# Optimization experiments

Measured on AMD Instinct MI355X. Metric: run time of the kernel, lower is better.

The kernel has to match this reference:

```python
import jax, jax.numpy as jnp
import numpy as np

# Dimensions
N = 50000      # num entities
FIN = 100      # entity input dim
NHID = 100     # per-head hidden dim
H = 2          # heads in first GAT layer
REL = 100      # relation embedding dim (== entity_out_dim[0])
E = 800000     # num edges
NRELS = 200    # num relations
B = 512        # batch of facts
HDIM = 100     # time-embedding dim (h_dim)
ALPHA = 0.2    # leaky relu slope


def l2norm(x, eps=1e-12):
    # torch F.normalize(p=2, dim=1)
    return x / jnp.maximum(jnp.linalg.norm(x, axis=1, keepdims=True), eps)


def gat_layer(x, edge0, edge1, rel_e, a, a2, num_nodes, concat):
    """KBAT SpGraphAttentionLayer (dropout omitted: eval mode).
    a: [out, 2*in + nrela]; a2: [out]. Aggregates into edge0 (edge[0])."""
    fin = x.shape[1]
    a_src, a_dst, a_rel = a[:, :fin], a[:, fin:2 * fin], a[:, 2 * fin:]
    # edge_m = a @ cat(h_src, h_dst, rel).T, computed without materializing the concat
    m = x[edge0] @ a_src.T + x[edge1] @ a_dst.T + rel_e @ a_rel.T  # [E, out]
    powers = -jax.nn.leaky_relu(m @ a2, ALPHA)                      # [E]
    e = jnp.exp(powers)                                             # [E]
    rowsum = jax.ops.segment_sum(e, edge0, num_segments=num_nodes) + 1e-12  # [N]
    h = jax.ops.segment_sum(e[:, None] * m, edge0, num_segments=num_nodes)  # [N, out]
    h = h / rowsum[:, None]
    return jax.nn.elu(h) if concat else h


def setup_inputs() -> dict:
    key = jax.random.key(0)
    ks = jax.random.split(key, 13)
    s = 0.08  # xavier-ish scale, keeps exp() of attention logits tame
    return {
        "entity_embeddings": jax.random.normal(ks[0], (N, FIN), jnp.float32) * s,
        "relation_table": jax.random.normal(ks[1], (NRELS, REL), jnp.float32) * s,
        "weight_t2": jax.random.normal(ks[2], (1, HDIM), jnp.float32),
        "bias_t2": jax.random.normal(ks[3], (1, HDIM), jnp.float32),
        "W_entities": jax.random.normal(ks[4], (FIN, H * NHID), jnp.float32) * s,
        "a_heads": jax.random.normal(ks[5], (H, NHID, 2 * FIN + REL), jnp.float32) * s,
        "a2_heads": jax.random.normal(ks[6], (H, NHID), jnp.float32) * s,
        "W_rel": jax.random.normal(ks[7], (REL, H * NHID), jnp.float32) * s,
        "a_out": jax.random.normal(ks[8], (H * NHID, 3 * H * NHID), jnp.float32) * s,
        "a2_out": jax.random.normal(ks[9], (H * NHID,), jnp.float32) * s,
        "edge_list": jax.random.randint(ks[10], (2, E), 0, N),
        "edge_type": jax.random.randint(ks[11], (E,), 0, NRELS),
        "batch_inputs": jax.random.randint(ks[12], (B, 4), 0, N),
    }


def reference(entity_embeddings, relation_table, weight_t2, bias_t2, W_entities,
              a_heads, a2_heads, W_rel, a_out, a2_out,
              edge_list, edge_type, batch_inputs):
    edge0, edge1 = edge_list[0], edge_list[1]
    # edge_embed = stack of relation_dict lookups
    edge_embed = relation_table[edge_type]                     # [E, REL]

    # SpGAT: multi-head attention layer 1 (concat=True, elu inside layer)
    heads = [gat_layer(entity_embeddings, edge0, edge1, edge_embed,
                       a_heads[i], a2_heads[i], N, True) for i in range(H)]
    x1 = jnp.concatenate(heads, axis=1)                        # [N, H*NHID]

    # NOTE: repo passes edge_embed (per-edge) as relation_embed -> [E, H*NHID]
    out_relation_1 = edge_embed @ W_rel                        # [E, H*NHID]
    edge_embed2 = out_relation_1[edge_type]                    # [E, H*NHID]

    x2 = jax.nn.elu(gat_layer(x1, edge0, edge1, edge_embed2, a_out, a2_out, N, False))

    # entity_embeddings.data = normalize(...).detach() happens before W_entities mm
    emb_norm = l2norm(entity_embeddings)

    # time embeddings: h_t rows are all identical -> index by heads is a broadcast
    t2 = batch_inputs[:, 3].astype(jnp.float32)                # [B]
    he = jnp.cos(t2[:, None] * weight_t2[0] + bias_t2[0])      # [B, HDIM]
    his_temp_embs = jnp.broadcast_to(he[:, None, :], (B, B, HDIM))

    mask = jnp.zeros((N,), x2.dtype).at[batch_inputs[:, 2]].set(1.0)
    entities_upgraded = emb_norm @ W_entities                  # [N, H*NHID]
    out = l2norm(entities_upgraded + mask[:, None] * x2)
    return out, his_temp_embs
```

## Files before the change

kernel.cpp:

```cpp
#include <hip/hip_runtime.h>
#include <hip/hip_fp16.h>
#include <stdint.h>

#define N_NODES 50000
#define FIN_D   100
#define E_EDGES 800000
#define NRELS   200
#define B_BATCH 512
#define HDIM    100

typedef _Float16 f16x8 __attribute__((ext_vector_type(8)));
typedef short    s16x8 __attribute__((ext_vector_type(8)));
typedef float    f32x4v __attribute__((ext_vector_type(4)));

__device__ __forceinline__ unsigned short f2bf(float f){
  unsigned int x = __builtin_bit_cast(unsigned int, f);
  unsigned int lsb = (x >> 16) & 1u;
  x += 0x7fffu + lsb;
  return (unsigned short)(x >> 16);
}
__device__ __forceinline__ float ldf(const void* p, size_t i, int fdt){
  if (fdt == 2) return __half2float(((const __half*)p)[i]);
  if (fdt == 1){ unsigned int x = ((unsigned int)((const unsigned short*)p)[i]) << 16;
                 return __builtin_bit_cast(float, x); }
  return ((const float*)p)[i];
}
__device__ __forceinline__ void stf(void* p, size_t i, float v, int fdt){
  if (fdt == 2) ((__half*)p)[i] = __float2half_rn(v);
  else if (fdt == 1) ((unsigned short*)p)[i] = f2bf(v);
  else ((float*)p)[i] = v;
}
__device__ __forceinline__ int ild(const void* p, size_t i, int i64){
  return i64 ? (int)((const long long*)p)[i] : ((const int*)p)[i];
}

__global__ void k_probe(const unsigned short* __restrict__ eh, const unsigned int* __restrict__ ew,
                        const unsigned int* __restrict__ elw, int* __restrict__ ifl){
  int t = threadIdx.x;
  int cF = 0, cB = 0, c32 = 0;
  #pragma unroll
  for (int j = 0; j < 4; ++j){
    unsigned short u = eh[4*t + j];
    {
      int e5 = (u >> 10) & 31, m = u & 1023;
      float v = (e5 == 0) ? ldexpf((float)m, -24) : ldexpf(1.f + m/1024.f, e5 - 15);
      if (v >= 0.004f && v <= 0.30f) cF++;
    }
    {
      unsigned int x = ((unsigned int)(u & 0x7FFF)) << 16;
      float v = __builtin_bit_cast(float, x);
      if (v >= 0.004f && v <= 0.30f) cB++;
    }
  }
  #pragma unroll
  for (int j = 0; j < 2; ++j){
    unsigned int w = ew[2*t + j] & 0x7FFFFFFFu;
    float v = __builtin_bit_cast(float, w);
    if (v >= 0.004f && v <= 0.30f) c32++;
  }
  for (int o = 1; o < 64; o <<= 1){
    cF += __shfl_xor(cF, o); cB += __shfl_xor(cB, o); c32 += __shfl_xor(c32, o);
  }
  int z = (elw[2*t + 1] == 0u) ? 1 : 0;
  unsigned long long mb = __ballot(z);
  if (t == 0){
    int fdt;
    if (c32 >= 96) fdt = 0;
    else fdt = (cB > cF) ? 1 : 2;
    ifl[1] = fdt;
    ifl[0] = (__popcll(mb) >= 60) ? 1 : 0;
  }
}

__global__ void k_init(int* __restrict__ midx, int* __restrict__ cnt,
                       int* __restrict__ nflag, int* __restrict__ fcnt){
  int i = blockIdx.x*256 + threadIdx.x;
  if (i < N_NODES){ midx[i] = -1; cnt[i] = 0; nflag[i] = 0; }
  if (i == 0) fcnt[0] = 0;
}
__global__ void k_mset(const void* __restrict__ binp, const int* __restrict__ ifl,
                       int* __restrict__ midx){
  int i = blockIdx.x*256 + threadIdx.x;
  if (i >= B_BATCH) return;
  midx[ild(binp, (size_t)i*4 + 2, ifl[0])] = i;
}

__global__ void k_tables(const void* __restrict__ ah, const void* __restrict__ aout,
                         const void* __restrict__ a2h, const void* __restrict__ a2o,
                         const void* __restrict__ went, const int* __restrict__ ifl,
                         float* __restrict__ aTs, float* __restrict__ aoTs,
                         float* __restrict__ a2f, float* __restrict__ a2of,
                         unsigned short* __restrict__ WswE, unsigned short* __restrict__ WswD,
                         unsigned short* __restrict__ WswD2){
  int i = blockIdx.x*256 + threadIdx.x;
  int fdt = ifl[1];
  if (i < 20000){ int k=i/200, t=i%200; aTs[i] = ldf(ah,(size_t)t*300+k,fdt); return; }
  i -= 20000;
  if (i < 40000){ int k=i/200, t=i%200; aoTs[i] = ldf(aout,(size_t)t*600+k,fdt); return; }
  i -= 40000;
  if (i < 200){ a2f[i] = ldf(a2h, i, fdt); return; }
  i -= 200;
  if (i < 200){ a2of[i] = ldf(a2o, i, fdt); return; }
  i -= 200;
  if (i < 2*26624){
    int tbl = i / 26624, r0 = i % 26624;
    int j = r0 & 7, l = (r0>>3) & 63, ks = (r0>>9) & 3, n = r0>>11;
    int k = ks*32 + (l>>4)*8 + j;
    int col = n*16 + (l&15);
    float v = 0.f;
    if (k < 100 && col < 200)
      v = tbl ? ldf(ah, (size_t)col*300 + 100 + k, fdt) : ldf(went, (size_t)k*200 + col, fdt);
    unsigned short h = (fdt == 2) ? __builtin_bit_cast(unsigned short, __float2half_rn(v)) : f2bf(v);
    (tbl ? WswD : WswE)[r0] = h;
    return;
  }
  i -= 2*26624;
  if (i < 46592){
    int j = i & 7, l = (i>>3) & 63, r = i >> 9;
    int ks = r % 7, n = r / 7;
    int k = ks*32 + (l>>4)*8 + j;
    int col = n*16 + (l&15);
    float v = (k < 200 && col < 200) ? ldf(aout, (size_t)col*600 + 200 + k, fdt) : 0.f;
    WswD2[i] = __builtin_bit_cast(unsigned short, __float2half_rn(v));
  }
}

__global__ __launch_bounds__(256)
void k_cvt_en(const void* __restrict__ ent, const int* __restrict__ ifl,
              float* __restrict__ ENf, float* __restrict__ invn){
  const int w = threadIdx.x >> 6, l = threadIdx.x & 63;
  const int n = blockIdx.x*4 + w;
  const int fdt = ifl[1];
  float x = 0.f, y = 0.f;
  if (l < 50){
    if (fdt == 0){
      float2 v = ((const float2*)ent)[(size_t)n*50 + l];
      x = v.x; y = v.y;
    } else if (fdt == 2){
      __half2 h = ((const __half2*)ent)[(size_t)n*50 + l];
      float2 v = __half22float2(h); x = v.x; y = v.y;
    } else {
      unsigned int u = ((const unsigned int*)ent)[(size_t)n*50 + l];
      x = __builtin_bit_cast(float, u << 16);
      y = __builtin_bit_cast(float, u & 0xFFFF0000u);
    }
    if (fdt != 0) ((float2*)ENf)[(size_t)n*50 + l] = make_float2(x, y);
  }
  float ss = x*x + y*y;
  #pragma unroll
  for (int o = 1; o < 64; o <<= 1) ss += __shfl_xor(ss, o);
  if (l == 0) invn[n] = 1.f / fmaxf(sqrtf(ss), 1e-12f);
}

__global__ __launch_bounds__(256)
void k_rel(const void* __restrict__ rtab, const void* __restrict__ ah, const void* __restrict__ aout,
           const void* __restrict__ wrel, const void* __restrict__ etype, const int* __restrict__ ifl,
           const float* __restrict__ a2f, const float* __restrict__ a2of,
           float* __restrict__ R1f, float* __restrict__ sR1,
           float* __restrict__ R2f, float* __restrict__ sR2){
  __shared__ float rt[100], mr[200], ml[200];
  const int bi = blockIdx.x, t = threadIdx.x, fdt = ifl[1];
  if (bi < 200){
    const int tt = bi;
    if (t < 100) rt[t] = ldf(rtab,(size_t)tt*100+t,fdt);
    __syncthreads();
    if (t < 200){
      float R = 0.f;
      for (int k = 0; k < 100; ++k) R += rt[k]*ldf(ah,(size_t)t*300+200+k,fdt);
      R1f[tt*200+t] = R; ml[t] = R*a2f[t];
    }
    __syncthreads();
    if (t < 64){
      float s = 0.f;
      for (int q = t; q < 100; q += 64) s += ml[q];
      for (int o = 1; o < 64; o <<= 1) s += __shfl_xor(s, o);
      if (t == 0) sR1[tt*2] = s;
    } else if (t < 128){
      int l = t - 64;
      float s = 0.f;
      for (int q = 100 + l; q < 200; q += 64) s += ml[q];
      for (int o = 1; o < 64; o <<= 1) s += __shfl_xor(s, o);
      if (l == 0) sR1[tt*2+1] = s;
    }
  } else {
    const int tt = bi - 200;
    const int g = ild(etype, tt, ifl[0]);
    if (t < 100) rt[t] = ldf(rtab,(size_t)g*100+t,fdt);
    __syncthreads();
    if (t < 200){
      float m = 0.f;
      for (int k = 0; k < 100; ++k) m += rt[k]*ldf(wrel,(size_t)k*200+t,fdt);
      mr[t] = m;
    }
    __syncthreads();
    if (t < 200){
      float R = 0.f;
      for (int k = 0; k < 200; ++k) R += mr[k]*ldf(aout,(size_t)t*600+400+k,fdt);
      R2f[tt*200+t] = R; ml[t] = R*a2of[t];
    }
    __syncthreads();
    if (t < 64){
      float s = 0.f;
      for (int q = t; q < 200; q += 64) s += ml[q];
      for (int o = 1; o < 64; o <<= 1) s += __shfl_xor(s, o);
      if (t == 0) sR2[tt] = s;
    }
  }
}

__global__ void k_count(const void* __restrict__ el, const int* __restrict__ ifl, int* __restrict__ cnt){
  int e = blockIdx.x*256 + threadIdx.x;
  if (e >= E_EDGES) return;
  atomicAdd(&cnt[ild(el, e, ifl[0])], 1);
}
__global__ __launch_bounds__(256)
void k_scanA(int* __restrict__ cnt, int* __restrict__ offs, int* __restrict__ bsum){
  __shared__ int bs[256];
  const int t = threadIdx.x, i = blockIdx.x*256 + t;
  int v = (i < N_NODES) ? cnt[i] : 0;
  bs[t] = v;
  __syncthreads();
  for (int o = 1; o < 256; o <<= 1){
    int u = (t >= o) ? bs[t-o] : 0;
    __syncthreads();
    bs[t] += u;
    __syncthreads();
  }
  if (i < N_NODES){ offs[i] = bs[t] - v; cnt[i] = 0; }
  if (t == 255) bsum[blockIdx.x] = bs[255];
}
__global__ __launch_bounds__(256)
void k_scanB(const int* __restrict__ bsum, int* __restrict__ bbase, int nblk){
  __shared__ int bs[256];
  const int t = threadIdx.x;
  int v = (t < nblk) ? bsum[t] : 0;
  bs[t] = v;
  __syncthreads();
  for (int o = 1; o < 256; o <<= 1){
    int u = (t >= o) ? bs[t-o] : 0;
    __syncthreads();
    bs[t] += u;
    __syncthreads();
  }
  if (t < nblk) bbase[t] = bs[t] - v;
}
__global__ __launch_bounds__(256)
void k_scanC(int* __restrict__ offs, const int* __restrict__ bbase){
  const int i = blockIdx.x*256 + threadIdx.x;
  if (i < N_NODES) offs[i] += bbase[i >> 8];
  if (i == N_NODES) offs[N_NODES] = E_EDGES;
}
__global__ void k_scatter(const void* __restrict__ el, const void* __restrict__ et,
                          const int* __restrict__ ifl, const int* __restrict__ offs,
                          int* __restrict__ fill, int* __restrict__ csr){
  int e = blockIdx.x*256 + threadIdx.x;
  if (e >= E_EDGES) return;
  int f = ifl[0];
  int a = ild(el, e, f);
  int pos = offs[a] + atomicAdd(&fill[a], 1);
  csr[pos] = ild(el, (size_t)E_EDGES + e, f) | (ild(et, e, f) << 16);
}

__global__ void k_flag(const void* __restrict__ binp, const int* __restrict__ ifl,
                       const int* __restrict__ offs, const int* __restrict__ csr,
                       int* __restrict__ nflag){
  const int i = blockIdx.x, t = threadIdx.x;
  const int n = ild(binp, (size_t)i*4 + 2, ifl[0]);
  if (t == 0) nflag[n] = 1;
  for (int j = offs[n] + t; j < offs[n+1]; j += 256) nflag[csr[j] & 0xFFFF] = 1;
}
__global__ void k_compact(const int* __restrict__ nflag, int* __restrict__ fcnt, int* __restrict__ flist){
  int i = blockIdx.x*256 + threadIdx.x;
  if (i < N_NODES && nflag[i]) flist[atomicAdd(fcnt, 1)] = i;
}

__device__ __forceinline__ void loadA(const void* ent, int fdt, int arow, int koff, uint4* a){
  if (fdt != 0){
    const unsigned short* E = (const unsigned short*)ent;
    #pragma unroll
    for (int ks = 0; ks < 3; ++ks){
      const uint2* p = (const uint2*)(E + (size_t)arow*100 + ks*32 + koff);
      uint2 u0 = p[0], u1 = p[1];
      a[ks] = make_uint4(u0.x, u0.y, u1.x, u1.y);
    }
    if (koff == 0){
      const uint2* p = (const uint2*)(E + (size_t)arow*100 + 96);
      uint2 u0 = p[0];
      a[3] = make_uint4(u0.x, u0.y, 0, 0);
    } else a[3] = make_uint4(0,0,0,0);
  } else {
    const float* E = (const float*)ent;
    #pragma unroll
    for (int ks = 0; ks < 3; ++ks){
      const uint4* p = (const uint4*)(E + (size_t)arow*100 + ks*32 + koff);
      uint4 lo = p[0], hi = p[1];
      a[ks].x = (lo.x>>16) | (lo.y & 0xFFFF0000u);
      a[ks].y = (lo.z>>16) | (lo.w & 0xFFFF0000u);
      a[ks].z = (hi.x>>16) | (hi.y & 0xFFFF0000u);
      a[ks].w = (hi.z>>16) | (hi.w & 0xFFFF0000u);
    }
    if (koff == 0){
      const uint4* p = (const uint4*)(E + (size_t)arow*100 + 96);
      uint4 lo = p[0];
      a[3] = make_uint4((lo.x>>16)|(lo.y&0xFFFF0000u), (lo.z>>16)|(lo.w&0xFFFF0000u), 0, 0);
    } else a[3] = make_uint4(0,0,0,0);
  }
}

__global__ __launch_bounds__(256)
void k_gemmD1(const void* __restrict__ ent, const int* __restrict__ ifl,
              const unsigned short* __restrict__ WswD, const float* __restrict__ a2f,
              __half* __restrict__ D1, float* __restrict__ sD)
{
  const int wid = threadIdx.x >> 6, l = threadIdx.x & 63;
  const int mt = blockIdx.x*4 + wid;
  if (mt >= 3125) return;
  const int fdt = ifl[1];
  const int arow = mt*16 + (l & 15);
  const int koff = (l >> 4)*8;
  uint4 a[4];
  loadA(ent, fdt, arow, koff, a);
  const int c15 = l & 15;
  const int rbase = mt*16 + (l >> 4)*4;
  float sh0[4] = {0,0,0,0}, sh1[4] = {0,0,0,0};
  const uint4* W4 = (const uint4*)WswD;
  #pragma unroll
  for (int n = 0; n < 13; ++n){
    const int col = n*16 + c15;
    f32x4v acc = {0.f, 0.f, 0.f, 0.f};
    if (fdt == 2){
      #pragma unroll
      for (int ks = 0; ks < 4; ++ks){
        uint4 w = W4[(n*4 + ks)*64 + l];
        acc = __builtin_amdgcn_mfma_f32_16x16x32_f16(
            __builtin_bit_cast(f16x8, a[ks]), __builtin_bit_cast(f16x8, w), acc, 0, 0, 0);
      }
    } else {
      #pragma unroll
      for (int ks = 0; ks < 4; ++ks){
        uint4 w = W4[(n*4 + ks)*64 + l];
        acc = __builtin_amdgcn_mfma_f32_16x16x32_bf16(
            __builtin_bit_cast(s16x8, a[ks]), __builtin_bit_cast(s16x8, w), acc, 0, 0, 0);
      }
    }
    const float a2v = (col < 200) ? a2f[col] : 0.f;
    #pragma unroll
    for (int r = 0; r < 4; ++r){
      float v = acc[r];
      if (col < 200) D1[(size_t)(rbase + r)*200 + col] = __float2half_rn(v);
      float m = v*a2v;
      if (col < 100) sh0[r] += m; else sh1[r] += m;
    }
  }
  #pragma unroll
  for (int o = 1; o < 16; o <<= 1){
    #pragma unroll
    for (int r = 0; r < 4; ++r){
      sh0[r] += __shfl_xor(sh0[r], o);
      sh1[r] += __shfl_xor(sh1[r], o);
    }
  }
  if (c15 == 0){
    #pragma unroll
    for (int r = 0; r < 4; ++r){
      sD[(size_t)(rbase + r)*2]     = sh0[r];
      sD[(size_t)(rbase + r)*2 + 1] = sh1[r];
    }
  }
}

__global__ __launch_bounds__(256)
void k_gemmEuf(const void* __restrict__ ent, const int* __restrict__ ifl,
               const unsigned short* __restrict__ WswE, const float* __restrict__ invn,
               const int* __restrict__ midx, const float* __restrict__ x2m, char* __restrict__ dout)
{
  const int wid = threadIdx.x >> 6, l = threadIdx.x & 63;
  const int mt = blockIdx.x*4 + wid;
  if (mt >= 3125) return;
  const int fdt = ifl[1];
  const int arow = mt*16 + (l & 15);
  const int koff = (l >> 4)*8;
  uint4 a[4];
  loadA(ent, fdt, arow, koff, a);
  const int c15 = l & 15;
  const int rbase = mt*16 + (l >> 4)*4;
  f32x4v acc[13];
  const uint4* W4 = (const uint4*)WswE;
  #pragma unroll
  for (int n = 0; n < 13; ++n){
    f32x4v c = {0.f, 0.f, 0.f, 0.f};
    if (fdt == 2){
      #pragma unroll
      for (int ks = 0; ks < 4; ++ks){
        uint4 w = W4[(n*4 + ks)*64 + l];
        c = __builtin_amdgcn_mfma_f32_16x16x32_f16(
            __builtin_bit_cast(f16x8, a[ks]), __builtin_bit_cast(f16x8, w), c, 0, 0, 0);
      }
    } else {
      #pragma unroll
      for (int ks = 0; ks < 4; ++ks){
        uint4 w = W4[(n*4 + ks)*64 + l];
        c = __builtin_amdgcn_mfma_f32_16x16x32_bf16(
            __builtin_bit_cast(s16x8, a[ks]), __builtin_bit_cast(s16x8, w), c, 0, 0, 0);
      }
    }
    acc[n] = c;
  }
  float iv[4]; int mi[4];
  #pragma unroll
  for (int r = 0; r < 4; ++r){ iv[r] = invn[rbase + r]; mi[r] = midx[rbase + r]; }
  float ssv[4] = {0,0,0,0};
  #pragma unroll
  for (int n = 0; n < 13; ++n){
    const int col = n*16 + c15;
    if (col < 200){
      #pragma unroll
      for (int r = 0; r < 4; ++r){
        float v = acc[n][r]*iv[r];
        if (mi[r] >= 0) v += x2m[(size_t)mi[r]*200 + col];
        acc[n][r] = v;
        ssv[r] += v*v;
      }
    }
  }
  #pragma unroll
  for (int o = 1; o < 16; o <<= 1){
    #pragma unroll
    for (int r = 0; r < 4; ++r) ssv[r] += __shfl_xor(ssv[r], o);
  }
  float rn[4];
  #pragma unroll
  for (int r = 0; r < 4; ++r) rn[r] = 1.f / fmaxf(sqrtf(ssv[r]), 1e-12f);
  #pragma unroll
  for (int n = 0; n < 13; ++n){
    const int col = n*16 + c15;
    if (col < 200){
      #pragma unroll
      for (int r = 0; r < 4; ++r)
        stf(dout, (size_t)(rbase + r)*200 + col, acc[n][r]*rn[r], fdt);
    }
  }
}

__global__ __launch_bounds__(256)
void k_D2g(const __half* __restrict__ x1, const int* __restrict__ flist, const int* __restrict__ fcnt,
           const unsigned short* __restrict__ WswD2, const float* __restrict__ a2of,
           __half* __restrict__ D2, float* __restrict__ sD2)
{
  const int wid = threadIdx.x >> 6, l = threadIdx.x & 63;
  const int mt = blockIdx.x*4 + wid;
  const int cnt = fcnt[0];
  if (mt*16 >= cnt) return;
  const int c15 = l & 15;
  const int koff = (l >> 4)*8;
  int ar = mt*16 + c15; if (ar >= cnt) ar = cnt - 1;
  const __half* xr = x1 + (size_t)flist[ar]*200;
  uint4 a[7];
  #pragma unroll
  for (int ks = 0; ks < 6; ++ks)
    a[ks] = *(const uint4*)(xr + ks*32 + koff);
  a[6] = (koff == 0) ? *(const uint4*)(xr + 192) : make_uint4(0,0,0,0);
  const int rbase = mt*16 + (l >> 4)*4;
  int ndR[4]; bool okR[4];
  #pragma unroll
  for (int r = 0; r < 4; ++r){
    int rr = rbase + r;
    okR[r] = rr < cnt;
    ndR[r] = flist[okR[r] ? rr : cnt - 1];
  }
  float sh[4] = {0,0,0,0};
  const uint4* W4 = (const uint4*)WswD2;
  #pragma unroll
  for (int n = 0; n < 13; ++n){
    const int col = n*16 + c15;
    f32x4v acc = {0.f, 0.f, 0.f, 0.f};
    #pragma unroll
    for (int ks = 0; ks < 7; ++ks){
      uint4 w = W4[(n*7 + ks)*64 + l];
      acc = __builtin_amdgcn_mfma_f32_16x16x32_f16(
          __builtin_bit_cast(f16x8, a[ks]), __builtin_bit_cast(f16x8, w), acc, 0, 0, 0);
    }
    const float a2v = (col < 200) ? a2of[col] : 0.f;
    #pragma unroll
    for (int r = 0; r < 4; ++r){
      float v = acc[r];
      if (col < 200 && okR[r]) D2[(size_t)ndR[r]*200 + col] = __float2half_rn(v);
      sh[r] += v*a2v;
    }
  }
  #pragma unroll
  for (int o = 1; o < 16; o <<= 1){
    #pragma unroll
    for (int r = 0; r < 4; ++r) sh[r] += __shfl_xor(sh[r], o);
  }
  if (c15 == 0){
    #pragma unroll
    for (int r = 0; r < 4; ++r)
      if (okR[r]) sD2[ndR[r]] = sh[r];
  }
}

__global__ __launch_bounds__(256)
void k_x1(const void* __restrict__ ent, const float* __restrict__ ENf, const int* __restrict__ ifl,
          const int* __restrict__ flist, const int* __restrict__ fcnt,
          const float* __restrict__ aTs, const float* __restrict__ a2f,
          const float* __restrict__ R1f, const float* __restrict__ sR1,
          const __half* __restrict__ D1, const float* __restrict__ sD,
          const int* __restrict__ offs, const int* __restrict__ csr, __half* __restrict__ x1)
{
  __shared__ float ml[200], sS2[2];
  const int bi = blockIdx.x, t = threadIdx.x;
  if (bi >= fcnt[0]) return;
  const int n = flist[bi];
  const int fdt = ifl[1];
  const float* ENp = (fdt == 0) ? (const float*)ent : ENf;
  float S = 0.f;
  if (t < 200){
    const float* ep = ENp + (size_t)n*100;
    for (int k = 0; k < 100; ++k) S += ep[k]*aTs[k*200+t];
    ml[t] = S*a2f[t];
  }
  __syncthreads();
  if (t < 64){
    float s = 0.f;
    for (int q = t; q < 100; q += 64) s += ml[q];
    for (int o = 1; o < 64; o <<= 1) s += __shfl_xor(s, o);
    if (t == 0) sS2[0] = s;
  } else if (t < 128){
    int l = t - 64;
    float s = 0.f;
    for (int q = 100 + l; q < 200; q += 64) s += ml[q];
    for (int o = 1; o < 64; o <<= 1) s += __shfl_xor(s, o);
    if (l == 0) sS2[1] = s;
  }
  __syncthreads();
  if (t >= 200) return;
  const int h = (t >= 100) ? 1 : 0;
  const float sS = sS2[h];
  float acc = 0.f, W = 0.f;
  const int beg = offs[n], end = offs[n+1];
  for (int j = beg; j < end; ++j){
    int pk = csr[j];
    int v = pk & 0xFFFF, tt = pk >> 16;
    float d = __half2float(D1[(size_t)v*200 + t]);
    float r = R1f[tt*200 + t];
    float p = sS + sD[(size_t)v*2 + h] + sR1[tt*2 + h];
    float lk = p > 0.f ? p : 0.2f*p;
    float w = expf(-lk);
    acc += w*(d + r); W += w;
  }
  float hh = (S*W + acc) / (W + 1e-12f);
  x1[(size_t)n*200 + t] = __float2half_rn(hh > 0.f ? hh : (expf(hh) - 1.f));
}

__global__ __launch_bounds__(256)
void k_x2m(const void* __restrict__ binp, const __half* __restrict__ x1, const float* __restrict__ aoTs,
           const float* __restrict__ a2of, const float* __restrict__ R2f, const float* __restrict__ sR2,
           const __half* __restrict__ D2, const float* __restrict__ sD2, const int* __restrict__ ifl,
           const int* __restrict__ offs, const int* __restrict__ csr, float* __restrict__ x2m)
{
  __shared__ float xn[200], ml[200], sS2[1];
  const int i = blockIdx.x, t = threadIdx.x;
  const int n = ild(binp, (size_t)i*4 + 2, ifl[0]);
  if (t < 200) xn[t] = __half2float(x1[(size_t)n*200 + t]);
  __syncthreads();
  float S = 0.f;
  if (t < 200){
    for (int k = 0; k < 200; ++k) S += xn[k]*aoTs[k*200+t];
    ml[t] = S*a2of[t];
  }
  __syncthreads();
  if (t < 64){
    float s = 0.f;
    for (int q = t; q < 200; q += 64) s += ml[q];
    for (int o = 1; o < 64; o <<= 1) s += __shfl_xor(s, o);
    if (t == 0) sS2[0] = s;
  }
  __syncthreads();
  if (t >= 200) return;
  const float sS = sS2[0];
  float acc = 0.f, W = 0.f;
  const int beg = offs[n], end = offs[n+1];
  for (int j = beg; j < end; ++j){
    int pk = csr[j];
    int v = pk & 0xFFFF, tt = pk >> 16;
    float d = __half2float(D2[(size_t)v*200 + t]);
    float r = R2f[tt*200 + t];
    float p = sS + sD2[v] + sR2[tt];
    float lk = p > 0.f ? p : 0.2f*p;
    float w = expf(-lk);
    acc += w*(d + r); W += w;
  }
  float hh = (S*W + acc) / (W + 1e-12f);
  x2m[(size_t)i*200 + t] = hh > 0.f ? hh : (expf(hh) - 1.f);
}

__global__ __launch_bounds__(256)
void k_his(const void* __restrict__ binp, const void* __restrict__ wt, const void* __restrict__ bt,
           const int* __restrict__ ifl, char* __restrict__ dout)
{
  __shared__ float he[100];
  __shared__ uint4 tile[50];
  const int i = blockIdx.x, t = threadIdx.x;
  const int fdt = ifl[1];
  const double t2 = (double)ild(binp, (size_t)i*4 + 3, ifl[0]);
  if (t < 100){
    double a = t2 * (double)ldf(wt, t, fdt) + (double)ldf(bt, t, fdt);
    he[t] = (float)cos(a);
  }
  __syncthreads();
  if (fdt == 0){
    float* tf = (float*)tile;
    if (t < 100) tf[t] = he[t];
    __syncthreads();
    uint4* out4 = (uint4*)(dout + 40000000 + (size_t)i*204800);
    for (int idx = t; idx < 12800; idx += 256) out4[idx] = tile[idx % 25];
  } else {
    unsigned short* th = (unsigned short*)tile;
    for (int j = t; j < 400; j += 256){
      float v = he[j % 100];
      th[j] = (fdt == 2) ? __builtin_bit_cast(unsigned short, __float2half_rn(v)) : f2bf(v);
    }
    __syncthreads();
    uint4* out4 = (uint4*)(dout + 20000000 + (size_t)i*102400);
    for (int idx = t; idx < 6400; idx += 256) out4[idx] = tile[idx % 50];
  }
}

extern "C" void kernel_launch(void* const* d_in, const int* in_sizes, int n_in,
                              void* d_out, int out_size, void* d_ws, size_t ws_size,
                              hipStream_t stream)
{
  (void)in_sizes; (void)n_in; (void)out_size; (void)ws_size;
  const void* ent  = d_in[0];
  const void* rtab = d_in[1];
  const void* w_t2 = d_in[2];
  const void* b_t2 = d_in[3];
  const void* Went = d_in[4];
  const void* ah   = d_in[5];
  const void* a2h  = d_in[6];
  const void* Wrel = d_in[7];
  const void* aout = d_in[8];
  const void* a2o  = d_in[9];
  const void* elist = d_in[10];
  const void* etype = d_in[11];
  const void* binp  = d_in[12];

  int* ifl = (int*)d_ws;

  char* dout = (char*)d_out;
  float* ENf = (float*)dout;
  __half* D12 = (__half*)(dout + 20000000);
  char* scr = dout + 40000000;
  size_t cur = 0;
  auto alloc = [&](size_t bytes) -> char* {
    char* p = scr + cur;
    cur = (cur + bytes + 255) & ~(size_t)255;
    return p;
  };
  __half* X1     = (__half*)alloc((size_t)N_NODES*200*2);
  int*   csr     = (int*)alloc((size_t)E_EDGES*4);
  int*   offs    = (int*)alloc((size_t)(N_NODES+1)*4);
  int*   cnt     = (int*)alloc((size_t)N_NODES*4);
  int*   midx    = (int*)alloc((size_t)N_NODES*4);
  int*   nflag   = (int*)alloc((size_t)N_NODES*4);
  int*   flist   = (int*)alloc((size_t)N_NODES*4);
  int*   fcnt    = (int*)alloc(256);
  int*   bsum    = (int*)alloc(1024);
  int*   bbase   = (int*)alloc(1024);
  float* invn    = (float*)alloc((size_t)N_NODES*4);
  float* x2m     = (float*)alloc((size_t)B_BATCH*200*4);
  float* aTs     = (float*)alloc((size_t)100*200*4);
  float* aoTs    = (float*)alloc((size_t)200*200*4);
  float* R1f     = (float*)alloc((size_t)200*200*4);
  float* R2f     = (float*)alloc((size_t)200*200*4);
  float* sD      = (float*)alloc((size_t)N_NODES*2*4);
  float* sD2     = (float*)alloc((size_t)N_NODES*4);
  float* sR1     = (float*)alloc((size_t)200*2*4);
  float* sR2     = (float*)alloc((size_t)200*4);
  float* a2f     = (float*)alloc((size_t)200*4);
  float* a2of    = (float*)alloc((size_t)200*4);
  unsigned short* WswE  = (unsigned short*)alloc((size_t)26624*2);
  unsigned short* WswD  = (unsigned short*)alloc((size_t)26624*2);
  unsigned short* WswD2 = (unsigned short*)alloc((size_t)46592*2);

  const int EB = (E_EDGES + 255) / 256;
  const int NB = (N_NODES + 255) / 256;
  const int NB1 = (N_NODES + 256) / 256;

  k_probe<<<dim3(1), dim3(64), 0, stream>>>((const unsigned short*)ent, (const unsigned int*)ent,
                                            (const unsigned int*)elist, ifl);
  k_init <<<dim3(NB), dim3(256), 0, stream>>>(midx, cnt, nflag, fcnt);
  k_mset <<<dim3(2), dim3(256), 0, stream>>>(binp, ifl, midx);
  k_tables<<<dim3(627), dim3(256), 0, stream>>>(ah, aout, a2h, a2o, Went, ifl,
                                                aTs, aoTs, a2f, a2of, WswE, WswD, WswD2);
  k_cvt_en<<<dim3(N_NODES/4), dim3(256), 0, stream>>>(ent, ifl, ENf, invn);
  k_rel  <<<dim3(400), dim3(256), 0, stream>>>(rtab, ah, aout, Wrel, etype, ifl,
                                               a2f, a2of, R1f, sR1, R2f, sR2);

  k_count<<<dim3(EB), dim3(256), 0, stream>>>(elist, ifl, cnt);
  k_scanA<<<dim3(NB), dim3(256), 0, stream>>>(cnt, offs, bsum);
  k_scanB<<<dim3(1), dim3(256), 0, stream>>>(bsum, bbase, NB);
  k_scanC<<<dim3(NB1), dim3(256), 0, stream>>>(offs, bbase);
  k_scatter<<<dim3(EB), dim3(256), 0, stream>>>(elist, etype, ifl, offs, cnt, csr);

  k_flag <<<dim3(B_BATCH), dim3(256), 0, stream>>>(binp, ifl, offs, csr, nflag);
  k_compact<<<dim3(NB), dim3(256), 0, stream>>>(nflag, fcnt, flist);

  k_gemmD1<<<dim3(782), dim3(256), 0, stream>>>(ent, ifl, WswD, a2f, D12, sD);
  k_x1 <<<dim3(N_NODES), dim3(256), 0, stream>>>(ent, ENf, ifl, flist, fcnt, aTs, a2f, R1f, sR1, D12, sD, offs, csr, X1);
  k_D2g<<<dim3(782), dim3(256), 0, stream>>>(X1, flist, fcnt, WswD2, a2of, D12, sD2);
  k_x2m<<<dim3(B_BATCH), dim3(256), 0, stream>>>(binp, X1, aoTs, a2of, R2f, sR2, D12, sD2, ifl, offs, csr, x2m);
  k_gemmEuf<<<dim3(782), dim3(256), 0, stream>>>(ent, ifl, WswE, invn, midx, x2m, dout);

  k_his<<<dim3(B_BATCH), dim3(256), 0, stream>>>(binp, w_t2, b_t2, ifl, dout);
}
```

Measured before the change: 491.2 us.

## Merge setup kernels, fuse flag/compact via atomics, and grid-stride k_x1

Folds the dtype probe into k_init, merges table construction and entity conversion into one k_setup launch, and adds pre-transposed relation weight tables so k_rel reads coalesced floats instead of strided converted loads. The scan drops its middle kernel by having each block reduce the preceding block sums itself. Frontier flagging and compaction are fused with atomicExch/atomicAdd, which removes a full-N pass. k_x1 now uses a grid-stride loop over the frontier instead of launching one block per node, most of which exited early. Together these cut launch count and idle blocks, at the cost of extra atomic contention and a nondeterministic frontier order.

```diff
diff --git a/kernel.cpp b/kernel.cpp
--- a/kernel.cpp
+++ b/kernel.cpp
@@ -34,66 +34,100 @@
   return i64 ? (int)((const long long*)p)[i] : ((const int*)p)[i];
 }
 
-__global__ void k_probe(const unsigned short* __restrict__ eh, const unsigned int* __restrict__ ew,
-                        const unsigned int* __restrict__ elw, int* __restrict__ ifl){
-  int t = threadIdx.x;
-  int cF = 0, cB = 0, c32 = 0;
-  #pragma unroll
-  for (int j = 0; j < 4; ++j){
-    unsigned short u = eh[4*t + j];
-    {
-      int e5 = (u >> 10) & 31, m = u & 1023;
-      float v = (e5 == 0) ? ldexpf((float)m, -24) : ldexpf(1.f + m/1024.f, e5 - 15);
-      if (v >= 0.004f && v <= 0.30f) cF++;
-    }
-    {
-      unsigned int x = ((unsigned int)(u & 0x7FFF)) << 16;
-      float v = __builtin_bit_cast(float, x);
-      if (v >= 0.004f && v <= 0.30f) cB++;
-    }
-  }
-  #pragma unroll
-  for (int j = 0; j < 2; ++j){
-    unsigned int w = ew[2*t + j] & 0x7FFFFFFFu;
-    float v = __builtin_bit_cast(float, w);
-    if (v >= 0.004f && v <= 0.30f) c32++;
-  }
-  for (int o = 1; o < 64; o <<= 1){
-    cF += __shfl_xor(cF, o); cB += __shfl_xor(cB, o); c32 += __shfl_xor(c32, o);
-  }
-  int z = (elw[2*t + 1] == 0u) ? 1 : 0;
-  unsigned long long mb = __ballot(z);
-  if (t == 0){
-    int fdt;
-    if (c32 >= 96) fdt = 0;
-    else fdt = (cB > cF) ? 1 : 2;
-    ifl[1] = fdt;
-    ifl[0] = (__popcll(mb) >= 60) ? 1 : 0;
-  }
-}
-
-__global__ void k_init(int* __restrict__ midx, int* __restrict__ cnt,
-                       int* __restrict__ nflag, int* __restrict__ fcnt){
+__global__ void k_init(const unsigned short* __restrict__ eh, const unsigned int* __restrict__ ew,
+                       const unsigned int* __restrict__ elw,
+                       int* __restrict__ midx, int* __restrict__ cnt,
+                       int* __restrict__ nflag, int* __restrict__ fcnt, int* __restrict__ ifl){
+  const int NB = (N_NODES + 255) / 256;
+  if ((int)blockIdx.x == NB){
+    int t = threadIdx.x;
+    if (t >= 64) return;
+    int cF = 0, cB = 0, c32 = 0;
+    #pragma unroll
+    for (int j = 0; j < 4; ++j){
+      unsigned short u = eh[4*t + j];
+      {
+        int e5 = (u >> 10) & 31, m = u & 1023;
+        float v = (e5 == 0) ? ldexpf((float)m, -24) : ldexpf(1.f + m/1024.f, e5 - 15);
+        if (v >= 0.004f && v <= 0.30f) cF++;
+      }
+      {
+        unsigned int x = ((unsigned int)(u & 0x7FFF)) << 16;
+        float v = __builtin_bit_cast(float, x);
+        if (v >= 0.004f && v <= 0.30f) cB++;
+      }
+    }
+    #pragma unroll
+    for (int j = 0; j < 2; ++j){
+      unsigned int w = ew[2*t + j] & 0x7FFFFFFFu;
+      float v = __builtin_bit_cast(float, w);
+      if (v >= 0.004f && v <= 0.30f) c32++;
+    }
+    for (int o = 1; o < 64; o <<= 1){
+      cF += __shfl_xor(cF, o); cB += __shfl_xor(cB, o); c32 += __shfl_xor(c32, o);
+    }
+    int z = (elw[2*t + 1] == 0u) ? 1 : 0;
+    unsigned long long mb = __ballot(z);
+    if (t == 0){
+      int fdt;
+      if (c32 >= 96) fdt = 0;
+      else fdt = (cB > cF) ? 1 : 2;
+      ifl[1] = fdt;
+      ifl[0] = (__popcll(mb) >= 60) ? 1 : 0;
+    }
+    return;
+  }
   int i = blockIdx.x*256 + threadIdx.x;
   if (i < N_NODES){ midx[i] = -1; cnt[i] = 0; nflag[i] = 0; }
   if (i == 0) fcnt[0] = 0;
 }
+
 __global__ void k_mset(const void* __restrict__ binp, const int* __restrict__ ifl,
-                       int* __restrict__ midx){
+                       int* __restrict__ midx, int* __restrict__ nflag,
+                       int* __restrict__ fcnt, int* __restrict__ flist){
   int i = blockIdx.x*256 + threadIdx.x;
   if (i >= B_BATCH) return;
-  midx[ild(binp, (size_t)i*4 + 2, ifl[0])] = i;
-}
-
-__global__ void k_tables(const void* __restrict__ ah, const void* __restrict__ aout,
-                         const void* __restrict__ a2h, const void* __restrict__ a2o,
-                         const void* __restrict__ went, const int* __restrict__ ifl,
-                         float* __restrict__ aTs, float* __restrict__ aoTs,
-                         float* __restrict__ a2f, float* __restrict__ a2of,
-                         unsigned short* __restrict__ WswE, unsigned short* __restrict__ WswD,
-                         unsigned short* __restrict__ WswD2){
-  int i = blockIdx.x*256 + threadIdx.x;
-  int fdt = ifl[1];
+  int n = ild(binp, (size_t)i*4 + 2, ifl[0]);
+  midx[n] = i;
+  if (atomicExch(&nflag[n], 1) == 0) flist[atomicAdd(fcnt, 1)] = n;
+}
+
+__global__ __launch_bounds__(256)
+void k_setup(const void* __restrict__ ent, const void* __restrict__ ah, const void* __restrict__ aout,
+             const void* __restrict__ a2h, const void* __restrict__ a2o, const void* __restrict__ went,
+             const int* __restrict__ ifl,
+             float* __restrict__ ENf, float* __restrict__ invn,
+             float* __restrict__ aTs, float* __restrict__ aoTs,
+             float* __restrict__ aTr, float* __restrict__ aoTr,
+             float* __restrict__ a2f, float* __restrict__ a2of,
+             unsigned short* __restrict__ WswE, unsigned short* __restrict__ WswD,
+             unsigned short* __restrict__ WswD2){
+  const int fdt = ifl[1];
+  if (blockIdx.x < 12500){
+    const int w = threadIdx.x >> 6, l = threadIdx.x & 63;
+    const int n = blockIdx.x*4 + w;
+    float x = 0.f, y = 0.f;
+    if (l < 50){
+      if (fdt == 0){
+        float2 v = ((const float2*)ent)[(size_t)n*50 + l];
+        x = v.x; y = v.y;
+      } else if (fdt == 2){
+        __half2 h = ((const __half2*)ent)[(size_t)n*50 + l];
+        float2 v = __half22float2(h); x = v.x; y = v.y;
+      } else {
+        unsigned int u = ((const unsigned int*)ent)[(size_t)n*50 + l];
+        x = __builtin_bit_cast(float, u << 16);
+        y = __builtin_bit_cast(float, u & 0xFFFF0000u);
+      }
+      if (fdt != 0) ((float2*)ENf)[(size_t)n*50 + l] = make_float2(x, y);
+    }
+    float ss = x*x + y*y;
+    #pragma unroll
+    for (int o = 1; o < 64; o <<= 1) ss += __shfl_xor(ss, o);
+    if (l == 0) invn[n] = 1.f / fmaxf(sqrtf(ss), 1e-12f);
+    return;
+  }
+  int i = (blockIdx.x - 12500)*256 + threadIdx.x;
   if (i < 20000){ int k=i/200, t=i%200; aTs[i] = ldf(ah,(size_t)t*300+k,fdt); return; }
   i -= 20000;
   if (i < 40000){ int k=i/200, t=i%200; aoTs[i] = ldf(aout,(size_t)t*600+k,fdt); return; }
@@ -122,39 +156,17 @@
     int col = n*16 + (l&15);
     float v = (k < 200 && col < 200) ? ldf(aout, (size_t)col*600 + 200 + k, fdt) : 0.f;
     WswD2[i] = __builtin_bit_cast(unsigned short, __float2half_rn(v));
-  }
-}
-
-__global__ __launch_bounds__(256)
-void k_cvt_en(const void* __restrict__ ent, const int* __restrict__ ifl,
-              float* __restrict__ ENf, float* __restrict__ invn){
-  const int w = threadIdx.x >> 6, l = threadIdx.x & 63;
-  const int n = blockIdx.x*4 + w;
-  const int fdt = ifl[1];
-  float x = 0.f, y = 0.f;
-  if (l < 50){
-    if (fdt == 0){
-      float2 v = ((const float2*)ent)[(size_t)n*50 + l];
-      x = v.x; y = v.y;
-    } else if (fdt == 2){
-      __half2 h = ((const __half2*)ent)[(size_t)n*50 + l];
-      float2 v = __half22float2(h); x = v.x; y = v.y;
-    } else {
-      unsigned int u = ((const unsigned int*)ent)[(size_t)n*50 + l];
-      x = __builtin_bit_cast(float, u << 16);
-      y = __builtin_bit_cast(float, u & 0xFFFF0000u);
-    }
-    if (fdt != 0) ((float2*)ENf)[(size_t)n*50 + l] = make_float2(x, y);
-  }
-  float ss = x*x + y*y;
-  #pragma unroll
-  for (int o = 1; o < 64; o <<= 1) ss += __shfl_xor(ss, o);
-  if (l == 0) invn[n] = 1.f / fmaxf(sqrtf(ss), 1e-12f);
-}
-
-__global__ __launch_bounds__(256)
-void k_rel(const void* __restrict__ rtab, const void* __restrict__ ah, const void* __restrict__ aout,
-           const void* __restrict__ wrel, const void* __restrict__ etype, const int* __restrict__ ifl,
+    return;
+  }
+  i -= 46592;
+  if (i < 20000){ int k=i/200, t=i%200; aTr[i] = ldf(ah,(size_t)t*300+200+k,fdt); return; }
+  i -= 20000;
+  if (i < 40000){ int k=i/200, t=i%200; aoTr[i] = ldf(aout,(size_t)t*600+400+k,fdt); return; }
+}
+
+__global__ __launch_bounds__(256)
+void k_rel(const void* __restrict__ rtab, const void* __restrict__ wrel, const void* __restrict__ etype,
+           const int* __restrict__ ifl, const float* __restrict__ aTr, const float* __restrict__ aoTr,
            const float* __restrict__ a2f, const float* __restrict__ a2of,
            float* __restrict__ R1f, float* __restrict__ sR1,
            float* __restrict__ R2f, float* __restrict__ sR2){
@@ -166,7 +178,7 @@
     __syncthreads();
     if (t < 200){
       float R = 0.f;
-      for (int k = 0; k < 100; ++k) R += rt[k]*ldf(ah,(size_t)t*300+200+k,fdt);
+      for (int k = 0; k < 100; ++k) R += rt[k]*aTr[k*200+t];
       R1f[tt*200+t] = R; ml[t] = R*a2f[t];
     }
     __syncthreads();
@@ -195,7 +207,7 @@
     __syncthreads();
     if (t < 200){
       float R = 0.f;
-      for (int k = 0; k < 200; ++k) R += mr[k]*ldf(aout,(size_t)t*600+400+k,fdt);
+      for (int k = 0; k < 200; ++k) R += mr[k]*aoTr[k*200+t];
       R2f[tt*200+t] = R; ml[t] = R*a2of[t];
     }
     __syncthreads();
@@ -230,24 +242,17 @@
   if (t == 255) bsum[blockIdx.x] = bs[255];
 }
 __global__ __launch_bounds__(256)
-void k_scanB(const int* __restrict__ bsum, int* __restrict__ bbase, int nblk){
-  __shared__ int bs[256];
-  const int t = threadIdx.x;
-  int v = (t < nblk) ? bsum[t] : 0;
-  bs[t] = v;
+void k_scanC(int* __restrict__ offs, const int* __restrict__ bsum){
+  __shared__ int part[4];
+  const int t = threadIdx.x, b = blockIdx.x;
+  int u = (t < b) ? bsum[t] : 0;
+  #pragma unroll
+  for (int o = 1; o < 64; o <<= 1) u += __shfl_xor(u, o);
+  if ((t & 63) == 0) part[t >> 6] = u;
   __syncthreads();
-  for (int o = 1; o < 256; o <<= 1){
-    int u = (t >= o) ? bs[t-o] : 0;
-    __syncthreads();
-    bs[t] += u;
-    __syncthreads();
-  }
-  if (t < nblk) bbase[t] = bs[t] - v;
-}
-__global__ __launch_bounds__(256)
-void k_scanC(int* __restrict__ offs, const int* __restrict__ bbase){
-  const int i = blockIdx.x*256 + threadIdx.x;
-  if (i < N_NODES) offs[i] += bbase[i >> 8];
+  const int base = part[0] + part[1] + part[2] + part[3];
+  const int i = b*256 + t;
+  if (i < N_NODES) offs[i] += base;
   if (i == N_NODES) offs[N_NODES] = E_EDGES;
 }
 __global__ void k_scatter(const void* __restrict__ el, const void* __restrict__ et,
@@ -263,15 +268,13 @@
 
 __global__ void k_flag(const void* __restrict__ binp, const int* __restrict__ ifl,
                        const int* __restrict__ offs, const int* __restrict__ csr,
-                       int* __restrict__ nflag){
+                       int* __restrict__ nflag, int* __restrict__ fcnt, int* __restrict__ flist){
   const int i = blockIdx.x, t = threadIdx.x;
   const int n = ild(binp, (size_t)i*4 + 2, ifl[0]);
-  if (t == 0) nflag[n] = 1;
-  for (int j = offs[n] + t; j < offs[n+1]; j += 256) nflag[csr[j] & 0xFFFF] = 1;
-}
-__global__ void k_compact(const int* __restrict__ nflag, int* __restrict__ fcnt, int* __restrict__ flist){
-  int i = blockIdx.x*256 + threadIdx.x;
-  if (i < N_NODES && nflag[i]) flist[atomicAdd(fcnt, 1)] = i;
+  for (int j = offs[n] + t; j < offs[n+1]; j += 256){
+    int v = csr[j] & 0xFFFF;
+    if (atomicExch(&nflag[v], 1) == 0) flist[atomicAdd(fcnt, 1)] = v;
+  }
 }
 
 __device__ __forceinline__ void loadA(const void* ent, int fdt, int arow, int koff, uint4* a){
@@ -509,48 +512,52 @@
           const int* __restrict__ offs, const int* __restrict__ csr, __half* __restrict__ x1)
 {
   __shared__ float ml[200], sS2[2];
-  const int bi = blockIdx.x, t = threadIdx.x;
-  if (bi >= fcnt[0]) return;
-  const int n = flist[bi];
+  const int t = threadIdx.x;
+  const int FC = fcnt[0];
   const int fdt = ifl[1];
   const float* ENp = (fdt == 0) ? (const float*)ent : ENf;
-  float S = 0.f;
-  if (t < 200){
-    const float* ep = ENp + (size_t)n*100;
-    for (int k = 0; k < 100; ++k) S += ep[k]*aTs[k*200+t];
-    ml[t] = S*a2f[t];
-  }
-  __syncthreads();
-  if (t < 64){
-    float s = 0.f;
-    for (int q = t; q < 100; q += 64) s += ml[q];
-    for (int o = 1; o < 64; o <<= 1) s += __shfl_xor(s, o);
-    if (t == 0) sS2[0] = s;
-  } else if (t < 128){
-    int l = t - 64;
-    float s = 0.f;
-    for (int q = 100 + l; q < 200; q += 64) s += ml[q];
-    for (int o = 1; o < 64; o <<= 1) s += __shfl_xor(s, o);
-    if (l == 0) sS2[1] = s;
-  }
-  __syncthreads();
-  if (t >= 200) return;
-  const int h = (t >= 100) ? 1 : 0;
-  const float sS = sS2[h];
-  float acc = 0.f, W = 0.f;
-  const int beg = offs[n], end = offs[n+1];
-  for (int j = beg; j < end; ++j){
-    int pk = csr[j];
-    int v = pk & 0xFFFF, tt = pk >> 16;
-    float d = __half2float(D1[(size_t)v*200 + t]);
-    float r = R1f[tt*200 + t];
-    float p = sS + sD[(size_t)v*2 + h] + sR1[tt*2 + h];
-    float lk = p > 0.f ? p : 0.2f*p;
-    float w = expf(-lk);
-    acc += w*(d + r); W += w;
-  }
-  float hh = (S*W + acc) / (W + 1e-12f);
-  x1[(size_t)n*200 + t] = __float2half_rn(hh > 0.f ? hh : (expf(hh) - 1.f));
+  for (int bi = blockIdx.x; bi < FC; bi += gridDim.x){
+    const int n = flist[bi];
+    float S = 0.f;
+    if (t < 200){
+      const float* ep = ENp + (size_t)n*100;
+      for (int k = 0; k < 100; ++k) S += ep[k]*aTs[k*200+t];
+      ml[t] = S*a2f[t];
+    }
+    __syncthreads();
+    if (t < 64){
+      float s = 0.f;
+      for (int q = t; q < 100; q += 64) s += ml[q];
+      for (int o = 1; o < 64; o <<= 1) s += __shfl_xor(s, o);
+      if (t == 0) sS2[0] = s;
+    } else if (t < 128){
+      int l = t - 64;
+      float s = 0.f;
+      for (int q = 100 + l; q < 200; q += 64) s += ml[q];
+      for (int o = 1; o < 64; o <<= 1) s += __shfl_xor(s, o);
+      if (l == 0) sS2[1] = s;
+    }
+    __syncthreads();
+    if (t < 200){
+      const int h = (t >= 100) ? 1 : 0;
+      const float sS = sS2[h];
+      float acc = 0.f, W = 0.f;
+      const int beg = offs[n], end = offs[n+1];
+      for (int j = beg; j < end; ++j){
+        int pk = csr[j];
+        int v = pk & 0xFFFF, tt = pk >> 16;
+        float d = __half2float(D1[(size_t)v*200 + t]);
+        float r = R1f[tt*200 + t];
+        float p = sS + sD[(size_t)v*2 + h] + sR1[tt*2 + h];
+        float lk = p > 0.f ? p : 0.2f*p;
+        float w = expf(-lk);
+        acc += w*(d + r); W += w;
+      }
+      float hh = (S*W + acc) / (W + 1e-12f);
+      x1[(size_t)n*200 + t] = __float2half_rn(hh > 0.f ? hh : (expf(hh) - 1.f));
+    }
+    __syncthreads();
+  }
 }
 
 __global__ __launch_bounds__(256)
@@ -667,11 +674,12 @@
   int*   flist   = (int*)alloc((size_t)N_NODES*4);
   int*   fcnt    = (int*)alloc(256);
   int*   bsum    = (int*)alloc(1024);
-  int*   bbase   = (int*)alloc(1024);
   float* invn    = (float*)alloc((size_t)N_NODES*4);
   float* x2m     = (float*)alloc((size_t)B_BATCH*200*4);
   float* aTs     = (float*)alloc((size_t)100*200*4);
   float* aoTs    = (float*)alloc((size_t)200*200*4);
+  float* aTr     = (float*)alloc((size_t)100*200*4);
+  float* aoTr    = (float*)alloc((size_t)200*200*4);
   float* R1f     = (float*)alloc((size_t)200*200*4);
   float* R2f     = (float*)alloc((size_t)200*200*4);
   float* sD      = (float*)alloc((size_t)N_NODES*2*4);
@@ -686,29 +694,25 @@
 
   const int EB = (E_EDGES + 255) / 256;
   const int NB = (N_NODES + 255) / 256;
-  const int NB1 = (N_NODES + 256) / 256;
-
-  k_probe<<<dim3(1), dim3(64), 0, stream>>>((const unsigned short*)ent, (const unsigned int*)ent,
-                                            (const unsigned int*)elist, ifl);
-  k_init <<<dim3(NB), dim3(256), 0, stream>>>(midx, cnt, nflag, fcnt);
-  k_mset <<<dim3(2), dim3(256), 0, stream>>>(binp, ifl, midx);
-  k_tables<<<dim3(627), dim3(256), 0, stream>>>(ah, aout, a2h, a2o, Went, ifl,
-                                                aTs, aoTs, a2f, a2of, WswE, WswD, WswD2);
-  k_cvt_en<<<dim3(N_NODES/4), dim3(256), 0, stream>>>(ent, ifl, ENf, invn);
-  k_rel  <<<dim3(400), dim3(256), 0, stream>>>(rtab, ah, aout, Wrel, etype, ifl,
+
+  k_init <<<dim3(NB + 1), dim3(256), 0, stream>>>((const unsigned short*)ent, (const unsigned int*)ent,
+                                                  (const unsigned int*)elist, midx, cnt, nflag, fcnt, ifl);
+  k_mset <<<dim3(2), dim3(256), 0, stream>>>(binp, ifl, midx, nflag, fcnt, flist);
+  k_setup<<<dim3(12500 + 861), dim3(256), 0, stream>>>(ent, ah, aout, a2h, a2o, Went, ifl,
+                                                       ENf, invn, aTs, aoTs, aTr, aoTr, a2f, a2of,
+                                                       WswE, WswD, WswD2);
+  k_rel  <<<dim3(400), dim3(256), 0, stream>>>(rtab, Wrel, etype, ifl, aTr, aoTr,
                                                a2f, a2of, R1f, sR1, R2f, sR2);
 
   k_count<<<dim3(EB), dim3(256), 0, stream>>>(elist, ifl, cnt);
   k_scanA<<<dim3(NB), dim3(256), 0, stream>>>(cnt, offs, bsum);
-  k_scanB<<<dim3(1), dim3(256), 0, stream>>>(bsum, bbase, NB);
-  k_scanC<<<dim3(NB1), dim3(256), 0, stream>>>(offs, bbase);
+  k_scanC<<<dim3(NB), dim3(256), 0, stream>>>(offs, bsum);
   k_scatter<<<dim3(EB), dim3(256), 0, stream>>>(elist, etype, ifl, offs, cnt, csr);
 
-  k_flag <<<dim3(B_BATCH), dim3(256), 0, stream>>>(binp, ifl, offs, csr, nflag);
-  k_compact<<<dim3(NB), dim3(256), 0, stream>>>(nflag, fcnt, flist);
+  k_flag <<<dim3(B_BATCH), dim3(256), 0, stream>>>(binp, ifl, offs, csr, nflag, fcnt, flist);
 
   k_gemmD1<<<dim3(782), dim3(256), 0, stream>>>(ent, ifl, WswD, a2f, D12, sD);
-  k_x1 <<<dim3(N_NODES), dim3(256), 0, stream>>>(ent, ENf, ifl, flist, fcnt, aTs, a2f, R1f, sR1, D12, sD, offs, csr, X1);
+  k_x1 <<<dim3(12288), dim3(256), 0, stream>>>(ent, ENf, ifl, flist, fcnt, aTs, a2f, R1f, sR1, D12, sD, offs, csr, X1);
   k_D2g<<<dim3(782), dim3(256), 0, stream>>>(X1, flist, fcnt, WswD2, a2of, D12, sD2);
   k_x2m<<<dim3(B_BATCH), dim3(256), 0, stream>>>(binp, X1, aoTs, a2of, R2f, sR2, D12, sD2, ifl, offs, csr, x2m);
   k_gemmEuf<<<dim3(782), dim3(256), 0, stream>>>(ent, ifl, WswE, invn, midx, x2m, dout);
```

Result: faster. 458.1 us (-6.7%).
